# Kernel optimization log

Measured on AMD Instinct MI355X. Metric: run time of the kernel, lower is better.

The kernel has to match this reference:

```python
import jax, jax.numpy as jnp
import numpy as np

EPS = 1e-9       # module's displacement/convergence epsilon
COS_EPS = 1e-8   # torch F.cosine_similarity eps (norms clamped at eps)
LN_EPS = 1e-5


def _safe_norm(sq):
    # sqrt with zero-safe gradient for exactly-zero (padded) vectors
    return jnp.where(sq > 0, jnp.sqrt(jnp.maximum(sq, 1e-30)), 0.0)


def _features(coords, n):
    """coords: [S, md] padded; n: true length (>=4). Returns [60] features."""
    S, md = coords.shape
    f32 = coords.dtype
    nf = n.astype(f32)
    idx_d = jnp.arange(S - 1)
    m = n - 1                       # number of valid deltas
    mf = m.astype(f32)
    dmask = idx_d < m
    dmaskf = dmask.astype(f32)

    deltas = (coords[1:] - coords[:-1]) * dmaskf[:, None]     # [S-1, md]
    dmags = _safe_norm(jnp.sum(deltas * deltas, axis=-1))      # [S-1]

    last = jnp.take(coords, n - 1, axis=0)
    total_disp = _safe_norm(jnp.sum((last - coords[0]) ** 2))
    path_len = jnp.sum(dmags)
    disp_ratio = total_disp / (path_len + EPS)
    n_steps_norm = nf / 10.0

    # consecutive cosine similarities / curvatures (valid count = n-2)
    na = jnp.maximum(dmags, COS_EPS)
    cos = jnp.sum(deltas[:-1] * deltas[1:], axis=-1) / (na[:-1] * na[1:])  # [S-2]
    idx_c = jnp.arange(S - 2)
    cmask = idx_c < (n - 2)
    cmaskf = cmask.astype(f32)
    ncf = (n - 2).astype(f32)
    curv = 1.0 - cos
    curv_m = jnp.where(cmask, curv, 0.0)
    mean_curv = jnp.sum(curv_m) / ncf
    max_curv = jnp.max(jnp.where(cmask, curv, -jnp.inf))
    min_curv = jnp.min(jnp.where(cmask, curv, jnp.inf))
    curv_var = jnp.sum(cmaskf * (curv - mean_curv) ** 2) / jnp.maximum(ncf - 1.0, 1.0)
    std_curv = jnp.where(ncf > 1.0, jnp.sqrt(jnp.maximum(curv_var, 1e-30)), 0.0)
    curv_range = max_curv - min_curv

    mean_cos = jnp.sum(jnp.where(cmask, cos, 0.0)) / ncf
    min_cos = jnp.min(jnp.where(cmask, cos, jnp.inf))
    dir_changes = jnp.sum(cmaskf * (cos < 0).astype(f32)) / jnp.maximum(ncf, 1.0)

    linearity = disp_ratio
    loop_score = 1.0 - total_disp / (path_len + EPS)

    half = m // 2
    fmaskf = (idx_d < half + 1).astype(f32)
    smaskf = ((idx_d >= half) & (idx_d < m)).astype(f32)
    first_half = jnp.sum(dmags * fmaskf) / (half + 1).astype(f32)
    second_half = jnp.sum(dmags * smaskf) / (m - half).astype(f32)
    convergence = (first_half - second_half) / (first_half + EPS)
    cascade = (second_half - first_half) / (first_half + EPS)

    # all-pairs cosine (the O(n^2) block) via one GEMM per sample
    cosmat = (deltas @ deltas.T) / (na[:, None] * na[None, :])  # [S-1, S-1]
    pmask = (idx_d[:, None] < idx_d[None, :]) & (idx_d[None, :] < m)
    npairs = mf * (mf - 1.0) / 2.0
    parallelism = jnp.sum(jnp.where(pmask, cosmat, 0.0)) / jnp.maximum(npairs, 1.0)

    mean_dm = path_len / mf
    dm_var = jnp.sum(dmaskf * (dmags - mean_dm) ** 2) / jnp.maximum(mf - 1.0, 1.0)
    std_dm = jnp.where(mf > 1.0, jnp.sqrt(jnp.maximum(dm_var, 1e-30)), 0.0)
    max_dm = jnp.max(jnp.where(dmask, dmags, -jnp.inf))
    jump = jnp.where(mean_dm > EPS, max_dm / mean_dm, 1.0)

    rmaskf = (jnp.arange(S) < n).astype(f32)
    cnt = nf * md
    mean_coord = jnp.sum(coords * rmaskf[:, None]) / cnt
    coord_var = jnp.sum(rmaskf[:, None] * (coords - mean_coord) ** 2) / (cnt - 1.0)
    std_coord = jnp.sqrt(jnp.maximum(coord_var, 1e-30))

    scalars = jnp.stack([
        total_disp, path_len, disp_ratio, n_steps_norm,
        mean_curv, max_curv, std_curv, curv_range,
        mean_cos, min_cos, dir_changes,
        linearity, loop_score, convergence, parallelism, jump, cascade,
        mean_dm, std_dm, mean_coord, std_coord,
    ])  # [21]
    padded_deltas = deltas[:3].reshape(-1)   # [30] (masked -> already zero-padded)
    padded_curvs = curv_m[:9]                # [9]
    return jnp.concatenate([scalars, padded_deltas, padded_curvs])  # [60]


def setup_inputs() -> dict:
    key = jax.random.key(0)
    ks = jax.random.split(key, 4)
    B, S, md, H = 32768, 48, 10, 48
    coords = jax.random.normal(ks[0], (B, S, md), dtype=jnp.float32)
    lengths = jax.random.randint(ks[1], (B,), 4, S + 1, dtype=jnp.int32)
    W = jax.random.normal(ks[2], (60, H), dtype=jnp.float32) * 0.1
    b = jax.random.normal(ks[3], (H,), dtype=jnp.float32) * 0.01
    ln_w = jnp.ones((H,), dtype=jnp.float32)
    ln_b = jnp.zeros((H,), dtype=jnp.float32)
    return {"coords": coords, "lengths": lengths, "W": W, "b": b, "ln_w": ln_w, "ln_b": ln_b}


def reference(coords, lengths, W, b, ln_w, ln_b):
    feats = jax.vmap(_features)(coords, lengths)          # [B, 60]
    h = feats @ W + b                                     # [B, 48]
    mu = jnp.mean(h, axis=-1, keepdims=True)
    var = jnp.mean((h - mu) ** 2, axis=-1, keepdims=True)
    h = (h - mu) / jnp.sqrt(var + LN_EPS) * ln_w + ln_b
    return jax.nn.gelu(h, approximate=False)              # dropout is identity at eval
```

## Files before the change

### kernel.cpp

```cpp
#include <hip/hip_runtime.h>
#include <math.h>

#define WPB 4

static __device__ __forceinline__ float wsum(float x){
#pragma unroll
  for (int off = 32; off > 0; off >>= 1) x += __shfl_xor(x, off, 64);
  return x;
}
static __device__ __forceinline__ float wmaxr(float x){
#pragma unroll
  for (int off = 32; off > 0; off >>= 1) x = fmaxf(x, __shfl_xor(x, off, 64));
  return x;
}
static __device__ __forceinline__ float wminr(float x){
#pragma unroll
  for (int off = 32; off > 0; off >>= 1) x = fminf(x, __shfl_xor(x, off, 64));
  return x;
}
static __device__ __forceinline__ float lane_bcastf(float x, int l){
  return __uint_as_float(__builtin_amdgcn_readlane(__float_as_uint(x), l));
}
static __device__ __forceinline__ float first_lanef(float x){
  return __uint_as_float(__builtin_amdgcn_readfirstlane(__float_as_uint(x)));
}

__global__ __launch_bounds__(WPB * 64)
void traj_kernel(const float* __restrict__ coords,
                 const int* __restrict__ lengths,
                 const float* __restrict__ W,
                 const float* __restrict__ bias,
                 const float* __restrict__ lnw,
                 const float* __restrict__ lnb,
                 float* __restrict__ out, int B)
{
  const int i = threadIdx.x & 63;
  const int b = blockIdx.x * WPB + (threadIdx.x >> 6);
  if (b >= B) return;

  const int n = __builtin_amdgcn_readfirstlane(lengths[b]);
  const int m = n - 1;
  const float* cp = coords + (size_t)b * 480;

  float c[10];
  if (i < 48) {
    const float2* p = reinterpret_cast<const float2*>(cp + i * 10);
    float2 v0 = p[0], v1 = p[1], v2 = p[2], v3 = p[3], v4 = p[4];
    c[0]=v0.x; c[1]=v0.y; c[2]=v1.x; c[3]=v1.y; c[4]=v2.x;
    c[5]=v2.y; c[6]=v3.x; c[7]=v3.y; c[8]=v4.x; c[9]=v4.y;
  } else {
#pragma unroll
    for (int k = 0; k < 10; k++) c[k] = 0.f;
  }

  const bool dact = (i < m);
  float d[10];
  float dsq = 0.f;
#pragma unroll
  for (int k = 0; k < 10; k++) {
    float cn = __shfl_down(c[k], 1, 64);
    float dd = dact ? (cn - c[k]) : 0.f;
    d[k] = dd;
    dsq = fmaf(dd, dd, dsq);
  }
  const float dmag = (dsq > 0.f) ? sqrtf(fmaxf(dsq, 1e-30f)) : 0.f;
  const float na   = fmaxf(dmag, 1e-8f);
  const float inv  = 1.0f / na;

  float dot = 0.f;
#pragma unroll
  for (int k = 0; k < 10; k++) {
    float dn = __shfl_down(d[k], 1, 64);
    dot = fmaf(d[k], dn, dot);
  }
  const float invn = __shfl_down(inv, 1, 64);
  const bool cact = (i < n - 2);
  const float cosv   = dot * inv * invn;
  const float curv   = 1.f - cosv;
  const float curv_m = cact ? curv : 0.f;
  const float cos_m  = cact ? cosv : 0.f;

  const int half = m >> 1;
  const float dmv = dmag;
  const float path_len = wsum(dmv);
  const float sum_dm2  = wsum(dmv * dmv);
  const float max_dm   = wmaxr(dmv);
  const float sum_f    = wsum((i < half + 1) ? dmv : 0.f);
  const float sum_s    = wsum((i >= half) ? dmv : 0.f);

  const float sum_cv  = wsum(curv_m);
  const float sum_cv2 = wsum(curv_m * curv_m);
  const float max_cv  = wmaxr(cact ? curv : -INFINITY);
  const float min_cv  = wminr(cact ? curv :  INFINITY);
  const float sum_cs  = wsum(cos_m);
  const float min_cs  = wminr(cact ? cosv :  INFINITY);
  const float sum_ng  = wsum((cact && cosv < 0.f) ? 1.f : 0.f);

  float Usq = 0.f;
#pragma unroll
  for (int k = 0; k < 10; k++) {
    float Uk = wsum(d[k] * inv);
    Usq = fmaf(Uk, Uk, Usq);
  }
  const float sum_uu = wsum(dsq * (inv * inv));

  float csl = 0.f, cs2l = 0.f;
  if (i < n) {
#pragma unroll
    for (int k = 0; k < 10; k++) { csl += c[k]; cs2l = fmaf(c[k], c[k], cs2l); }
  }
  const float sum_c  = wsum(csl);
  const float sum_c2 = wsum(cs2l);

  float tsql = 0.f;
#pragma unroll
  for (int k = 0; k < 10; k++) {
    float c0 = lane_bcastf(c[k], 0);
    float t = c[k] - c0;
    tsql = fmaf(t, t, tsql);
  }
  const float tsq = lane_bcastf(tsql, m);
  const float total_disp = (tsq > 0.f) ? sqrtf(fmaxf(tsq, 1e-30f)) : 0.f;

  const float EPSf = 1e-9f;
  const float nf = (float)n, mf = (float)m, ncf = (float)(n - 2);
  const float disp_ratio = total_disp / (path_len + EPSf);
  const float mean_cv = sum_cv / ncf;
  const float cv_var  = (sum_cv2 - ncf * mean_cv * mean_cv) / fmaxf(ncf - 1.f, 1.f);
  const float std_cv  = sqrtf(fmaxf(cv_var, 1e-30f));
  const float mean_cs = sum_cs / ncf;
  const float dirchg  = sum_ng / fmaxf(ncf, 1.f);
  const float fh = sum_f / (float)(half + 1);
  const float sh = sum_s / (float)(m - half);
  const float conv = (fh - sh) / (fh + EPSf);
  const float casc = (sh - fh) / (fh + EPSf);
  const float npairs = mf * (mf - 1.f) * 0.5f;
  const float par = 0.5f * (Usq - sum_uu) / fmaxf(npairs, 1.f);
  const float mean_dm = path_len / mf;
  const float dm_var = (sum_dm2 - mf * mean_dm * mean_dm) / fmaxf(mf - 1.f, 1.f);
  const float std_dm = sqrtf(fmaxf(dm_var, 1e-30f));
  const float jump = (mean_dm > EPSf) ? (max_dm / mean_dm) : 1.f;
  const float cnt = nf * 10.f;
  const float mean_co = sum_c / cnt;
  const float co_var = (sum_c2 - cnt * mean_co * mean_co) / (cnt - 1.f);
  const float std_co = sqrtf(fmaxf(co_var, 1e-30f));

  float feat[60];
  feat[0]  = first_lanef(total_disp);
  feat[1]  = first_lanef(path_len);
  feat[2]  = first_lanef(disp_ratio);
  feat[3]  = nf * 0.1f;
  feat[4]  = first_lanef(mean_cv);
  feat[5]  = first_lanef(max_cv);
  feat[6]  = first_lanef(std_cv);
  feat[7]  = first_lanef(max_cv - min_cv);
  feat[8]  = first_lanef(mean_cs);
  feat[9]  = first_lanef(min_cs);
  feat[10] = first_lanef(dirchg);
  feat[11] = feat[2];
  feat[12] = 1.f - feat[2];
  feat[13] = first_lanef(conv);
  feat[14] = first_lanef(par);
  feat[15] = first_lanef(jump);
  feat[16] = first_lanef(casc);
  feat[17] = first_lanef(mean_dm);
  feat[18] = first_lanef(std_dm);
  feat[19] = first_lanef(mean_co);
  feat[20] = first_lanef(std_co);
#pragma unroll
  for (int r = 0; r < 3; r++)
#pragma unroll
    for (int k = 0; k < 10; k++)
      feat[21 + r * 10 + k] = lane_bcastf(d[k], r);
#pragma unroll
  for (int r = 0; r < 9; r++)
    feat[51 + r] = lane_bcastf(curv_m, r);

  float h = 0.f;
  if (i < 48) {
    h = bias[i];
#pragma unroll
    for (int f = 0; f < 60; ++f) h = fmaf(feat[f], W[f * 48 + i], h);
  }

  const float hm = (i < 48) ? h : 0.f;
  const float s1 = wsum(hm);
  const float s2 = wsum(hm * hm);
  const float mu  = s1 * (1.f / 48.f);
  const float var = s2 * (1.f / 48.f) - mu * mu;

  if (i < 48) {
    float x = (h - mu) / sqrtf(var + 1e-5f) * lnw[i] + lnb[i];
    float g = 0.5f * x * (1.f + erff(x * 0.70710678118654752f));
    out[(size_t)b * 48 + i] = g;
  }
}

extern "C" void kernel_launch(void* const* d_in, const int* in_sizes, int n_in,
                              void* d_out, int out_size, void* d_ws, size_t ws_size,
                              hipStream_t stream)
{
  const float* coords = (const float*)d_in[0];
  const int*   lengths= (const int*)d_in[1];
  const float* W      = (const float*)d_in[2];
  const float* bias   = (const float*)d_in[3];
  const float* lnw    = (const float*)d_in[4];
  const float* lnb    = (const float*)d_in[5];
  float* out = (float*)d_out;

  const int B = in_sizes[1];
  const int blocks = (B + WPB - 1) / WPB;
  traj_kernel<<<blocks, WPB * 64, 0, stream>>>(coords, lengths, W, bias, lnw, lnb, out, B);
}
```

Measured before the change: 150.0 us.

## Use DPP wave reductions, fast intrinsics, reload neighbors, and transposed W

```diff
diff --git a/kernel.cpp b/kernel.cpp
--- a/kernel.cpp
+++ b/kernel.cpp
@@ -3,32 +3,58 @@
 
 #define WPB 4
 
+template<int CTRL, int RM>
+static __device__ __forceinline__ float dppadd(float x){
+  int t = __builtin_amdgcn_update_dpp(0, __float_as_int(x), CTRL, RM, 0xf, true);
+  return x + __int_as_float(t);
+}
+template<int CTRL, int RM>
+static __device__ __forceinline__ float dppmax(float x){
+  int t = __builtin_amdgcn_update_dpp(__float_as_int(x), __float_as_int(x), CTRL, RM, 0xf, false);
+  return fmaxf(x, __int_as_float(t));
+}
+template<int CTRL, int RM>
+static __device__ __forceinline__ float dppmin(float x){
+  int t = __builtin_amdgcn_update_dpp(__float_as_int(x), __float_as_int(x), CTRL, RM, 0xf, false);
+  return fminf(x, __int_as_float(t));
+}
+static __device__ __forceinline__ float rl(float x, int l){
+  return __uint_as_float(__builtin_amdgcn_readlane(__float_as_uint(x), l));
+}
 static __device__ __forceinline__ float wsum(float x){
-#pragma unroll
-  for (int off = 32; off > 0; off >>= 1) x += __shfl_xor(x, off, 64);
-  return x;
-}
-static __device__ __forceinline__ float wmaxr(float x){
-#pragma unroll
-  for (int off = 32; off > 0; off >>= 1) x = fmaxf(x, __shfl_xor(x, off, 64));
-  return x;
-}
-static __device__ __forceinline__ float wminr(float x){
-#pragma unroll
-  for (int off = 32; off > 0; off >>= 1) x = fminf(x, __shfl_xor(x, off, 64));
-  return x;
-}
-static __device__ __forceinline__ float lane_bcastf(float x, int l){
-  return __uint_as_float(__builtin_amdgcn_readlane(__float_as_uint(x), l));
-}
-static __device__ __forceinline__ float first_lanef(float x){
-  return __uint_as_float(__builtin_amdgcn_readfirstlane(__float_as_uint(x)));
-}
-
+  x = dppadd<0x111,0xf>(x);
+  x = dppadd<0x112,0xf>(x);
+  x = dppadd<0x114,0xf>(x);
+  x = dppadd<0x118,0xf>(x);
+  x = dppadd<0x142,0xa>(x);
+  x = dppadd<0x143,0xc>(x);
+  return rl(x, 63);
+}
+static __device__ __forceinline__ float wmax(float x){
+  x = dppmax<0x111,0xf>(x); x = dppmax<0x112,0xf>(x);
+  x = dppmax<0x114,0xf>(x); x = dppmax<0x118,0xf>(x);
+  x = dppmax<0x142,0xa>(x); x = dppmax<0x143,0xc>(x);
+  return rl(x, 63);
+}
+static __device__ __forceinline__ float wmin(float x){
+  x = dppmin<0x111,0xf>(x); x = dppmin<0x112,0xf>(x);
+  x = dppmin<0x114,0xf>(x); x = dppmin<0x118,0xf>(x);
+  x = dppmin<0x142,0xa>(x); x = dppmin<0x143,0xc>(x);
+  return rl(x, 63);
+}
+static __device__ __forceinline__ float frcp(float x){ return __builtin_amdgcn_rcpf(x); }
+static __device__ __forceinline__ float fsqrt(float x){ return __builtin_amdgcn_sqrtf(x); }
+
+__global__ void transpose_w(const float* __restrict__ W, float* __restrict__ Wt){
+  int idx = blockIdx.x * 256 + threadIdx.x;
+  if (idx < 60 * 48) { int f = idx / 48, j = idx - f * 48; Wt[j * 60 + f] = W[idx]; }
+}
+
+template<bool USEWT>
 __global__ __launch_bounds__(WPB * 64)
 void traj_kernel(const float* __restrict__ coords,
                  const int* __restrict__ lengths,
-                 const float* __restrict__ W,
+                 const float* __restrict__ Wsrc,
                  const float* __restrict__ bias,
                  const float* __restrict__ lnw,
                  const float* __restrict__ lnb,
@@ -42,7 +68,7 @@
   const int m = n - 1;
   const float* cp = coords + (size_t)b * 480;
 
-  float c[10];
+  float c[10], cnx[10];
   if (i < 48) {
     const float2* p = reinterpret_cast<const float2*>(cp + i * 10);
     float2 v0 = p[0], v1 = p[1], v2 = p[2], v3 = p[3], v4 = p[4];
@@ -52,20 +78,27 @@
 #pragma unroll
     for (int k = 0; k < 10; k++) c[k] = 0.f;
   }
+  if (i < 47) {
+    const float2* p = reinterpret_cast<const float2*>(cp + (i + 1) * 10);
+    float2 v0 = p[0], v1 = p[1], v2 = p[2], v3 = p[3], v4 = p[4];
+    cnx[0]=v0.x; cnx[1]=v0.y; cnx[2]=v1.x; cnx[3]=v1.y; cnx[4]=v2.x;
+    cnx[5]=v2.y; cnx[6]=v3.x; cnx[7]=v3.y; cnx[8]=v4.x; cnx[9]=v4.y;
+  } else {
+#pragma unroll
+    for (int k = 0; k < 10; k++) cnx[k] = 0.f;
+  }
 
   const bool dact = (i < m);
-  float d[10];
-  float dsq = 0.f;
-#pragma unroll
-  for (int k = 0; k < 10; k++) {
-    float cn = __shfl_down(c[k], 1, 64);
-    float dd = dact ? (cn - c[k]) : 0.f;
+  float d[10]; float dsq = 0.f;
+#pragma unroll
+  for (int k = 0; k < 10; k++) {
+    float dd = dact ? (cnx[k] - c[k]) : 0.f;
     d[k] = dd;
     dsq = fmaf(dd, dd, dsq);
   }
-  const float dmag = (dsq > 0.f) ? sqrtf(fmaxf(dsq, 1e-30f)) : 0.f;
+  const float dmag = (dsq > 0.f) ? fsqrt(fmaxf(dsq, 1e-30f)) : 0.f;
   const float na   = fmaxf(dmag, 1e-8f);
-  const float inv  = 1.0f / na;
+  const float inv  = frcp(na);
 
   float dot = 0.f;
 #pragma unroll
@@ -75,26 +108,22 @@
   }
   const float invn = __shfl_down(inv, 1, 64);
   const bool cact = (i < n - 2);
-  const float cosv   = dot * inv * invn;
-  const float curv   = 1.f - cosv;
-  const float curv_m = cact ? curv : 0.f;
-  const float cos_m  = cact ? cosv : 0.f;
+  const float cosv  = dot * inv * invn;
+  const float cos_m = cact ? cosv : 0.f;
 
   const int half = m >> 1;
-  const float dmv = dmag;
-  const float path_len = wsum(dmv);
-  const float sum_dm2  = wsum(dmv * dmv);
-  const float max_dm   = wmaxr(dmv);
-  const float sum_f    = wsum((i < half + 1) ? dmv : 0.f);
-  const float sum_s    = wsum((i >= half) ? dmv : 0.f);
-
-  const float sum_cv  = wsum(curv_m);
-  const float sum_cv2 = wsum(curv_m * curv_m);
-  const float max_cv  = wmaxr(cact ? curv : -INFINITY);
-  const float min_cv  = wminr(cact ? curv :  INFINITY);
-  const float sum_cs  = wsum(cos_m);
-  const float min_cs  = wminr(cact ? cosv :  INFINITY);
-  const float sum_ng  = wsum((cact && cosv < 0.f) ? 1.f : 0.f);
+  const float path_len = wsum(dmag);
+  const float sum_dm2  = wsum(dsq);
+  const float max_dm   = wmax(dmag);
+  const float sum_f    = wsum((i <= half) ? dmag : 0.f);
+  const float dm_half  = __uint_as_float(__builtin_amdgcn_readlane(__float_as_uint(dmag), half));
+  const float sum_s    = path_len + dm_half - sum_f;
+
+  const float sum_cos  = wsum(cos_m);
+  const float sum_cos2 = wsum(cos_m * cos_m);
+  const float max_cos  = wmax(cact ? cosv : -INFINITY);
+  const float min_cos  = wmin(cact ? cosv :  INFINITY);
+  const float sum_ng   = wsum((cact && cosv < 0.f) ? 1.f : 0.f);
 
   float Usq = 0.f;
 #pragma unroll
@@ -115,82 +144,99 @@
   float tsql = 0.f;
 #pragma unroll
   for (int k = 0; k < 10; k++) {
-    float c0 = lane_bcastf(c[k], 0);
+    float c0 = rl(c[k], 0);
     float t = c[k] - c0;
     tsql = fmaf(t, t, tsql);
   }
-  const float tsq = lane_bcastf(tsql, m);
-  const float total_disp = (tsq > 0.f) ? sqrtf(fmaxf(tsq, 1e-30f)) : 0.f;
+  const float tdq = __uint_as_float(__builtin_amdgcn_readlane(__float_as_uint(tsql), m));
+  const float total_disp = (tdq > 0.f) ? fsqrt(fmaxf(tdq, 1e-30f)) : 0.f;
 
   const float EPSf = 1e-9f;
   const float nf = (float)n, mf = (float)m, ncf = (float)(n - 2);
-  const float disp_ratio = total_disp / (path_len + EPSf);
-  const float mean_cv = sum_cv / ncf;
-  const float cv_var  = (sum_cv2 - ncf * mean_cv * mean_cv) / fmaxf(ncf - 1.f, 1.f);
-  const float std_cv  = sqrtf(fmaxf(cv_var, 1e-30f));
-  const float mean_cs = sum_cs / ncf;
-  const float dirchg  = sum_ng / fmaxf(ncf, 1.f);
-  const float fh = sum_f / (float)(half + 1);
-  const float sh = sum_s / (float)(m - half);
-  const float conv = (fh - sh) / (fh + EPSf);
-  const float casc = (sh - fh) / (fh + EPSf);
+  const float rncf = frcp(ncf);
+  const float disp_ratio = total_disp * frcp(path_len + EPSf);
+  const float sum_cv  = ncf - sum_cos;
+  const float mean_cv = sum_cv * rncf;
+  const float sum_cv2 = fmaf(-2.f, sum_cos, ncf) + sum_cos2;
+  const float cv_var  = (sum_cv2 - ncf * mean_cv * mean_cv) * frcp(fmaxf(ncf - 1.f, 1.f));
+  const float std_cv  = fsqrt(fmaxf(cv_var, 1e-30f));
+  const float max_cv  = 1.f - min_cos;
+  const float cv_rng  = max_cos - min_cos;
+  const float mean_cs = sum_cos * rncf;
+  const float dirchg  = sum_ng * rncf;
+  const float fh = sum_f * frcp((float)(half + 1));
+  const float sh = sum_s * frcp((float)(m - half));
+  const float conv = (fh - sh) * frcp(fh + EPSf);
   const float npairs = mf * (mf - 1.f) * 0.5f;
-  const float par = 0.5f * (Usq - sum_uu) / fmaxf(npairs, 1.f);
-  const float mean_dm = path_len / mf;
-  const float dm_var = (sum_dm2 - mf * mean_dm * mean_dm) / fmaxf(mf - 1.f, 1.f);
-  const float std_dm = sqrtf(fmaxf(dm_var, 1e-30f));
-  const float jump = (mean_dm > EPSf) ? (max_dm / mean_dm) : 1.f;
+  const float par = (Usq - sum_uu) * 0.5f * frcp(npairs);
+  const float mean_dm = path_len * frcp(mf);
+  const float dm_var = (sum_dm2 - mf * mean_dm * mean_dm) * frcp(mf - 1.f);
+  const float std_dm = fsqrt(fmaxf(dm_var, 1e-30f));
+  const float jump = (mean_dm > EPSf) ? max_dm * frcp(mean_dm) : 1.f;
   const float cnt = nf * 10.f;
-  const float mean_co = sum_c / cnt;
-  const float co_var = (sum_c2 - cnt * mean_co * mean_co) / (cnt - 1.f);
-  const float std_co = sqrtf(fmaxf(co_var, 1e-30f));
+  const float mean_co = sum_c * frcp(cnt);
+  const float co_var = (sum_c2 - cnt * mean_co * mean_co) * frcp(cnt - 1.f);
+  const float std_co = fsqrt(fmaxf(co_var, 1e-30f));
 
   float feat[60];
-  feat[0]  = first_lanef(total_disp);
-  feat[1]  = first_lanef(path_len);
-  feat[2]  = first_lanef(disp_ratio);
+  feat[0]  = total_disp;
+  feat[1]  = path_len;
+  feat[2]  = disp_ratio;
   feat[3]  = nf * 0.1f;
-  feat[4]  = first_lanef(mean_cv);
-  feat[5]  = first_lanef(max_cv);
-  feat[6]  = first_lanef(std_cv);
-  feat[7]  = first_lanef(max_cv - min_cv);
-  feat[8]  = first_lanef(mean_cs);
-  feat[9]  = first_lanef(min_cs);
-  feat[10] = first_lanef(dirchg);
-  feat[11] = feat[2];
-  feat[12] = 1.f - feat[2];
-  feat[13] = first_lanef(conv);
-  feat[14] = first_lanef(par);
-  feat[15] = first_lanef(jump);
-  feat[16] = first_lanef(casc);
-  feat[17] = first_lanef(mean_dm);
-  feat[18] = first_lanef(std_dm);
-  feat[19] = first_lanef(mean_co);
-  feat[20] = first_lanef(std_co);
+  feat[4]  = mean_cv;
+  feat[5]  = max_cv;
+  feat[6]  = std_cv;
+  feat[7]  = cv_rng;
+  feat[8]  = mean_cs;
+  feat[9]  = min_cos;
+  feat[10] = dirchg;
+  feat[11] = disp_ratio;
+  feat[12] = 1.f - disp_ratio;
+  feat[13] = conv;
+  feat[14] = par;
+  feat[15] = jump;
+  feat[16] = -conv;
+  feat[17] = mean_dm;
+  feat[18] = std_dm;
+  feat[19] = mean_co;
+  feat[20] = std_co;
 #pragma unroll
   for (int r = 0; r < 3; r++)
 #pragma unroll
     for (int k = 0; k < 10; k++)
-      feat[21 + r * 10 + k] = lane_bcastf(d[k], r);
+      feat[21 + r * 10 + k] = rl(d[k], r);
+  const float curv_m = cact ? (1.f - cosv) : 0.f;
 #pragma unroll
   for (int r = 0; r < 9; r++)
-    feat[51 + r] = lane_bcastf(curv_m, r);
+    feat[51 + r] = rl(curv_m, r);
 
   float h = 0.f;
   if (i < 48) {
     h = bias[i];
-#pragma unroll
-    for (int f = 0; f < 60; ++f) h = fmaf(feat[f], W[f * 48 + i], h);
+    if (USEWT) {
+      const float4* wr = reinterpret_cast<const float4*>(Wsrc + i * 60);
+#pragma unroll
+      for (int q = 0; q < 15; ++q) {
+        float4 w = wr[q];
+        h = fmaf(feat[4 * q + 0], w.x, h);
+        h = fmaf(feat[4 * q + 1], w.y, h);
+        h = fmaf(feat[4 * q + 2], w.z, h);
+        h = fmaf(feat[4 * q + 3], w.w, h);
+      }
+    } else {
+#pragma unroll
+      for (int f = 0; f < 60; ++f) h = fmaf(feat[f], Wsrc[f * 48 + i], h);
+    }
   }
 
   const float hm = (i < 48) ? h : 0.f;
   const float s1 = wsum(hm);
   const float s2 = wsum(hm * hm);
   const float mu  = s1 * (1.f / 48.f);
-  const float var = s2 * (1.f / 48.f) - mu * mu;
+  const float var = fmaf(-mu, mu, s2 * (1.f / 48.f));
 
   if (i < 48) {
-    float x = (h - mu) / sqrtf(var + 1e-5f) * lnw[i] + lnb[i];
+    float x = (h - mu) * __builtin_amdgcn_rsqf(var + 1e-5f) * lnw[i] + lnb[i];
     float g = 0.5f * x * (1.f + erff(x * 0.70710678118654752f));
     out[(size_t)b * 48 + i] = g;
   }
@@ -210,5 +256,12 @@
 
   const int B = in_sizes[1];
   const int blocks = (B + WPB - 1) / WPB;
-  traj_kernel<<<blocks, WPB * 64, 0, stream>>>(coords, lengths, W, bias, lnw, lnb, out, B);
-}
+
+  if (ws_size >= (size_t)(60 * 48 * sizeof(float))) {
+    float* Wt = (float*)d_ws;
+    transpose_w<<<12, 256, 0, stream>>>(W, Wt);
+    traj_kernel<true><<<blocks, WPB * 64, 0, stream>>>(coords, lengths, Wt, bias, lnw, lnb, out, B);
+  } else {
+    traj_kernel<false><<<blocks, WPB * 64, 0, stream>>>(coords, lengths, W, bias, lnw, lnb, out, B);
+  }
+}
```

Result: faster. 126.4 us (-15.7%).
